# Kernel tuning notes

Hardware: AMD Instinct MI355X
Metric: run time of the kernel (lower is better)

## Reference

```python
import jax, jax.numpy as jnp
import numpy as np

B, T, F = 16, 4096, 80      # batch, frames, mel bins
C = 512                     # conv channels
ZD, ZN = 64, 512            # codebook dim / size
YD, YN = 128, 128           # speaker embed dim / count
K = 5                       # kernel size
SLOPE = 0.2                 # leaky relu negative slope


def conv1d(x, w, b):
    # x: [B,Cin,T], w: [Cout,Cin,K], 'same' padding, stride 1
    pad = (w.shape[-1] - 1) // 2
    y = jax.lax.conv_general_dilated(x, w, (1,), [(pad, pad)],
                                     dimension_numbers=('NCH', 'OIH', 'NCH'))
    return y + b[None, :, None]


def convT1(x, w, b):
    # torch ConvTranspose1d(stride=1, padding=(K-1)//2) == conv with spatially
    # flipped, in/out-swapped kernel. w: [Cin, Cout, K]
    wc = jnp.flip(w, -1).transpose(1, 0, 2)  # -> [Cout, Cin, K]
    return conv1d(x, wc, b)


def ln_c(x, g, b, eps=1e-5):
    # layer norm over channel axis, per (batch, time) position
    m = jnp.mean(x, 1, keepdims=True)
    v = jnp.var(x, 1, keepdims=True)
    return (x - m) * jax.lax.rsqrt(v + eps) * g[None, :, None] + b[None, :, None]


def _forward(x, y, enc_w1, enc_b1, enc_g1, enc_bt1, enc_w2, enc_b2, enc_g2, enc_bt2,
             enc_w3, enc_b3, enc_g3, enc_bt3, mlp_w, mlp_b, codebook, spk_emb,
             dec_w1, dec_b1, dec_g1, dec_bt1, dec_w2, dec_b2, dec_g2, dec_bt2,
             dec_w3, dec_b3):
    xc = x.transpose(0, 2, 1)                                    # [B,F,T]
    # Conditions: normalized speaker embedding lookup
    spk = spk_emb / jnp.linalg.norm(spk_emb, axis=1, keepdims=True)
    ye = spk[y].transpose(0, 2, 1)                               # [B,YD,T]
    # encoder: Conv1d -> LayerNorm(channel) -> LeakyReLU, x3, then 1x1 conv to z_dim
    h = jax.nn.leaky_relu(ln_c(conv1d(xc, enc_w1, enc_b1), enc_g1, enc_bt1), SLOPE)
    h = jax.nn.leaky_relu(ln_c(conv1d(h, enc_w2, enc_b2), enc_g2, enc_bt2), SLOPE)
    h = jax.nn.leaky_relu(ln_c(conv1d(h, enc_w3, enc_b3), enc_g3, enc_bt3), SLOPE)
    z = conv1d(h, mlp_w, mlp_b)                                  # [B,ZD,T]
    # vector quantizer (eval path): cdist^2 -> argmin -> gather
    zt = z.transpose(0, 2, 1)                                    # [B,T,ZD]
    zf = zt.reshape(-1, ZD)                                      # [B*T,ZD]
    d = (jnp.sum(zf * zf, axis=1, keepdims=True)
         + jnp.sum(codebook * codebook, axis=1)
         - 2.0 * zf @ codebook.T)                                # [B*T,ZN]
    idx = jnp.argmin(d, axis=1)
    z_vq = codebook[idx].reshape(zt.shape).transpose(0, 2, 1)    # [B,ZD,T]
    # decoder: (concat y -> ConvT -> LayerNorm -> GLU) x2, then concat y -> ConvT
    def glu_layer(h, w, b, g, bt):
        h = jnp.concatenate([h, ye], axis=1)
        h = ln_c(convT1(h, w, b), g, bt)
        a, gate = jnp.split(h, 2, axis=1)
        return a * jax.nn.sigmoid(gate)
    h = glu_layer(z_vq, dec_w1, dec_b1, dec_g1, dec_bt1)
    h = glu_layer(h, dec_w2, dec_b2, dec_g2, dec_bt2)
    h = jnp.concatenate([h, ye], axis=1)
    xhat = convT1(h, dec_w3, dec_b3)                             # [B,F,T]
    return xhat.transpose(0, 2, 1)                               # [B,T,F]


def setup_inputs() -> dict:
    key = jax.random.key(0)
    ks = jax.random.split(key, 16)
    def n(k, shape, sc=0.05):
        return jax.random.normal(k, shape, jnp.float32) * sc
    return {
        "x": jax.random.normal(ks[0], (B, T, F), jnp.float32),
        "y": jax.random.randint(ks[1], (B, T), 0, YN),
        "enc_w1": n(ks[2], (C, F, K)), "enc_b1": jnp.zeros(C), "enc_g1": jnp.ones(C), "enc_bt1": jnp.zeros(C),
        "enc_w2": n(ks[3], (C, C, K)), "enc_b2": jnp.zeros(C), "enc_g2": jnp.ones(C), "enc_bt2": jnp.zeros(C),
        "enc_w3": n(ks[4], (C, C, K)), "enc_b3": jnp.zeros(C), "enc_g3": jnp.ones(C), "enc_bt3": jnp.zeros(C),
        "mlp_w": n(ks[5], (ZD, C, 1)), "mlp_b": jnp.zeros(ZD),
        "codebook": jax.random.normal(ks[6], (ZN, ZD), jnp.float32),
        "spk_emb": jax.random.normal(ks[7], (YN, YD), jnp.float32),
        "dec_w1": n(ks[8], (ZD + YD, 2 * C, K)), "dec_b1": jnp.zeros(2 * C), "dec_g1": jnp.ones(2 * C), "dec_bt1": jnp.zeros(2 * C),
        "dec_w2": n(ks[9], (C + YD, 2 * C, K)), "dec_b2": jnp.zeros(2 * C), "dec_g2": jnp.ones(2 * C), "dec_bt2": jnp.zeros(2 * C),
        "dec_w3": n(ks[10], (C + YD, F, K)), "dec_b3": jnp.zeros(F),
    }


def reference(x, y, enc_w1, enc_b1, enc_g1, enc_bt1, enc_w2, enc_b2, enc_g2, enc_bt2,
              enc_w3, enc_b3, enc_g3, enc_bt3, mlp_w, mlp_b, codebook, spk_emb,
              dec_w1, dec_b1, dec_g1, dec_bt1, dec_w2, dec_b2, dec_g2, dec_bt2,
              dec_w3, dec_b3):
    return _forward(x, y, enc_w1, enc_b1, enc_g1, enc_bt1, enc_w2, enc_b2, enc_g2, enc_bt2,
                    enc_w3, enc_b3, enc_g3, enc_bt3, mlp_w, mlp_b, codebook, spk_emb,
                    dec_w1, dec_b1, dec_g1, dec_bt1, dec_w2, dec_b2, dec_g2, dec_bt2,
                    dec_w3, dec_b3)
```

## Files before the change

### kernel.cpp

```cpp
#include <hip/hip_runtime.h>
#include <hip/hip_bf16.h>
#include <cmath>

#define T_LEN 4096
#define BATCH 16
typedef __hip_bfloat16 bf16;
typedef unsigned short u16;
typedef float f32x4 __attribute__((ext_vector_type(4)));
typedef short s16x8 __attribute__((ext_vector_type(8)));

__device__ __forceinline__ float ldx(const void* p, int dt, size_t i) {
    return dt ? __bfloat162float(((const bf16*)p)[i]) : ((const float*)p)[i];
}
__device__ __forceinline__ void stx(void* p, int dt, size_t i, float v) {
    if (dt) ((bf16*)p)[i] = __float2bfloat16(v);
    else ((float*)p)[i] = v;
}
__device__ __forceinline__ u16 f2b(float v) {
    bf16 h = __float2bfloat16(v);
    return *(u16*)&h;
}
__device__ __forceinline__ float b2f(u16 u) {
    return __bfloat162float(*(const bf16*)&u);
}

__global__ void detect_kernel(const float* __restrict__ x, int* __restrict__ flag) {
    __shared__ int s[256];
    int tid = threadIdx.x;
    int bad = 0;
    for (int i = tid; i < 2048; i += 256) {
        float v = x[i];
        if (!(fabsf(v) < 1e30f)) bad = 1;
    }
    s[tid] = bad;
    __syncthreads();
    for (int off = 128; off > 0; off >>= 1) {
        if (tid < off) s[tid] |= s[tid + off];
        __syncthreads();
    }
    if (tid == 0) *flag = s[0];
}

__global__ void spk_norm_kernel(const int* __restrict__ dflag,
                                const void* __restrict__ spk,
                                float* __restrict__ out) {
    const int f = *dflag;
    int s = blockIdx.x, d = threadIdx.x;
    float v = ldx(spk, f, (size_t)s * 128 + d);
    __shared__ float red[128];
    red[d] = v * v;
    __syncthreads();
    for (int off = 64; off > 0; off >>= 1) {
        if (d < off) red[d] += red[d + off];
        __syncthreads();
    }
    float rs = rsqrtf(red[0]);
    out[s * 128 + d] = v * rs;
}

__global__ void repack_kernel(const int* __restrict__ dflag,
                              const void* __restrict__ src, int wmode,
                              int Cout, int Cin, int K, int ocp, int Cinp,
                              bf16* __restrict__ dsthi, bf16* __restrict__ dstlo) {
    const int F = *dflag;
    size_t total = (size_t)K * ocp * Cinp;
    size_t stride = (size_t)gridDim.x * 256;
    for (size_t i = (size_t)blockIdx.x * 256 + threadIdx.x; i < total; i += stride) {
        int k = (int)(i / ((size_t)ocp * Cinp));
        int r = (int)(i % ((size_t)ocp * Cinp));
        int oc = r / Cinp, ic = r % Cinp;
        float v = 0.f;
        if (oc < Cout && ic < Cin) {
            size_t off = wmode ? (((size_t)ic * Cout + oc) * K + (K - 1 - k))
                               : (((size_t)oc * Cin + ic) * K + k);
            v = ldx(src, F, off);
        }
        bf16 h = __float2bfloat16(v);
        dsthi[i] = h;
        if (dstlo) dstlo[i] = __float2bfloat16(v - __bfloat162float(h));
    }
}

__global__ void xprep_kernel(const int* __restrict__ dflag,
                             const void* __restrict__ x, int b0,
                             bf16* __restrict__ xp) {
    const int F = *dflag;
    int b = blockIdx.y;
    int t = blockIdx.x * 256 + threadIdx.x;
    size_t src = ((size_t)(b0 + b) * T_LEN + t) * 80;
    u16* row = (u16*)xp + ((size_t)b * T_LEN + t) * 192;
    for (int c4 = 0; c4 < 96; c4 += 4) {
        ushort4 h, l;
        u16* hp = (u16*)&h;
        u16* lp = (u16*)&l;
        for (int j = 0; j < 4; j++) {
            int c = c4 + j;
            float v = (c < 80) ? ldx(x, F, src + c) : 0.f;
            u16 hb = f2b(v);
            hp[j] = hb;
            lp[j] = f2b(v - b2f(hb));
        }
        *(ushort4*)&row[c4] = h;
        *(ushort4*)&row[96 + c4] = l;
    }
}

__global__ void ye_kernel(const int* __restrict__ y, int b0,
                          const float* __restrict__ spk_n,
                          bf16* __restrict__ D1, bf16* __restrict__ D2,
                          bf16* __restrict__ D3) {
    int b = blockIdx.y;
    int t = blockIdx.x * 256 + threadIdx.x;
    int idx = y[(size_t)(b0 + b) * T_LEN + t];
    const float* s = spk_n + (size_t)idx * 128;
    size_t r = (size_t)b * T_LEN + t;
    u16* p1 = (u16*)D1 + r * 192 + 64;
    u16* p2 = (u16*)D2 + r * 640 + 512;
    u16* p3 = (u16*)D3 + r * 640 + 512;
    for (int d4 = 0; d4 < 128; d4 += 4) {
        float4 v = *(const float4*)&s[d4];
        ushort4 h;
        h.x = f2b(v.x); h.y = f2b(v.y); h.z = f2b(v.z); h.w = f2b(v.w);
        *(ushort4*)&p1[d4] = h;
        *(ushort4*)&p2[d4] = h;
        *(ushort4*)&p3[d4] = h;
    }
}

template <int KK>
__global__ __launch_bounds__(256) void conv_mfma(
    const int* __restrict__ dflag,
    const bf16* __restrict__ act, int RS, int loOff, int aloMode, int Cinp,
    const bf16* __restrict__ whi, const bf16* __restrict__ wlo, int wloMode,
    const void* __restrict__ bias,
    void* __restrict__ outp, int odt, int oRS, int ocMax, int boff) {
    constexpr int PAD = (KK - 1) / 2;
    constexpr int SROWS = 128 + KK - 1;
    const int F = *dflag;
    const bool useALo = (aloMode == 1) || (aloMode == 2 && F == 0);
    const bool useWLo = (wloMode == 2 && F == 0) && (wlo != nullptr);
    const int ocp = gridDim.y << 6;
    const int t0 = blockIdx.x * 128;
    const int oc0 = blockIdx.y * 64;
    const int b = blockIdx.z;
    const int tid = threadIdx.x;
    const int lane = tid & 63;
    const int wid = tid >> 6;
    const int l16 = lane & 15;
    const int q8 = (lane >> 4) * 8;
    const int quad = lane >> 4;

    __shared__ __align__(16) bf16 sA[2 * SROWS * 40];
    __shared__ __align__(16) bf16 sB[KK * 64 * 40];

    f32x4 acc[2][4];
#pragma unroll
    for (int i = 0; i < 2; i++)
#pragma unroll
        for (int j = 0; j < 4; j++) acc[i][j] = (f32x4){0.f, 0.f, 0.f, 0.f};

    const int nch = Cinp >> 5;
    for (int ch = 0; ch < nch; ch++) {
        const int ic0 = ch << 5;
        for (int g = tid; g < SROWS * 8; g += 256) {
            int row = g >> 3, c4 = (g & 7) << 2;
            int t = t0 - PAD + row;
            ushort4 v = make_ushort4(0, 0, 0, 0);
            ushort4 vl = make_ushort4(0, 0, 0, 0);
            if (t >= 0 && t < T_LEN) {
                const u16* src = (const u16*)act + ((size_t)b * T_LEN + t) * RS + ic0 + c4;
                v = *(const ushort4*)src;
                if (useALo) vl = *(const ushort4*)(src + loOff);
            }
            *(ushort4*)&sA[row * 40 + c4] = v;
            if (useALo) *(ushort4*)&sA[(SROWS + row) * 40 + c4] = vl;
        }
        for (int g = tid; g < KK * 512; g += 256) {
            int tap = g >> 9;
            int rr = g & 511;
            int ocr = rr >> 3, c4 = (rr & 7) << 2;
            const u16* src = (const u16*)whi +
                             ((size_t)tap * ocp + oc0 + ocr) * Cinp + ic0 + c4;
            *(ushort4*)&sB[(tap * 64 + ocr) * 40 + c4] = *(const ushort4*)src;
        }
        __syncthreads();

#pragma unroll
        for (int tap = 0; tap < KK; tap++) {
            s16x8 bfr[4];
#pragma unroll
            for (int ni = 0; ni < 4; ni++)
                bfr[ni] = *(const s16x8*)&sB[(tap * 64 + ni * 16 + l16) * 40 + q8];
#pragma unroll
            for (int mi = 0; mi < 2; mi++) {
                int row = wid * 32 + mi * 16 + l16 + tap;
                s16x8 a = *(const s16x8*)&sA[row * 40 + q8];
#pragma unroll
                for (int ni = 0; ni < 4; ni++)
                    acc[mi][ni] = __builtin_amdgcn_mfma_f32_16x16x32_bf16(
                        a, bfr[ni], acc[mi][ni], 0, 0, 0);
                if (useALo) {
                    s16x8 al = *(const s16x8*)&sA[(SROWS + row) * 40 + q8];
#pragma unroll
                    for (int ni = 0; ni < 4; ni++)
                        acc[mi][ni] = __builtin_amdgcn_mfma_f32_16x16x32_bf16(
                            al, bfr[ni], acc[mi][ni], 0, 0, 0);
                }
            }
        }
        if (useWLo) {
            __syncthreads();
            for (int g = tid; g < KK * 512; g += 256) {
                int tap = g >> 9;
                int rr = g & 511;
                int ocr = rr >> 3, c4 = (rr & 7) << 2;
                const u16* src = (const u16*)wlo +
                                 ((size_t)tap * ocp + oc0 + ocr) * Cinp + ic0 + c4;
                *(ushort4*)&sB[(tap * 64 + ocr) * 40 + c4] = *(const ushort4*)src;
            }
            __syncthreads();
#pragma unroll
            for (int tap = 0; tap < KK; tap++) {
                s16x8 bfr[4];
#pragma unroll
                for (int ni = 0; ni < 4; ni++)
                    bfr[ni] = *(const s16x8*)&sB[(tap * 64 + ni * 16 + l16) * 40 + q8];
#pragma unroll
                for (int mi = 0; mi < 2; mi++) {
                    int row = wid * 32 + mi * 16 + l16 + tap;
                    s16x8 a = *(const s16x8*)&sA[row * 40 + q8];
#pragma unroll
                    for (int ni = 0; ni < 4; ni++)
                        acc[mi][ni] = __builtin_amdgcn_mfma_f32_16x16x32_bf16(
                            a, bfr[ni], acc[mi][ni], 0, 0, 0);
                }
            }
        }
        __syncthreads();
    }

#pragma unroll
    for (int ni = 0; ni < 4; ni++) {
        int oc = oc0 + ni * 16 + l16;
        if (oc >= ocMax) continue;
        float bv = ldx(bias, F, oc);
#pragma unroll
        for (int mi = 0; mi < 2; mi++) {
#pragma unroll
            for (int r = 0; r < 4; r++) {
                int t = t0 + wid * 32 + mi * 16 + quad * 4 + r;
                float v = acc[mi][ni][r] + bv;
                size_t off = ((size_t)(b + boff) * T_LEN + t) * (size_t)oRS + oc;
                if (odt == 0) ((float*)outp)[off] = v;
                else if (odt == 1) ((bf16*)outp)[off] = __float2bfloat16(v);
                else stx(outp, F, off, v);
            }
        }
    }
}

__global__ __launch_bounds__(256) void ln_lrelu(
    const int* __restrict__ dflag, const float* __restrict__ Fin,
    bf16* __restrict__ E, const void* __restrict__ g, const void* __restrict__ bt) {
    const int Fl = *dflag;
    int b = blockIdx.y;
    int t = blockIdx.x * 4 + (threadIdx.x >> 6);
    int lane = threadIdx.x & 63;
    const float* row = Fin + ((size_t)b * T_LEN + t) * 512 + lane * 8;
    float vv[8];
    *(float4*)&vv[0] = *(const float4*)row;
    *(float4*)&vv[4] = *(const float4*)(row + 4);
    float s = 0.f, s2 = 0.f;
#pragma unroll
    for (int j = 0; j < 8; j++) { s += vv[j]; s2 += vv[j] * vv[j]; }
    for (int m = 32; m; m >>= 1) {
        s += __shfl_xor(s, m);
        s2 += __shfl_xor(s2, m);
    }
    float mean = s / 512.f;
    float var = s2 / 512.f - mean * mean;
    float rstd = rsqrtf(var + 1e-5f);
    u16* eo = (u16*)E + ((size_t)b * T_LEN + t) * 1024 + lane * 8;
    ushort4 h[2], l[2];
#pragma unroll
    for (int j = 0; j < 8; j++) {
        int c = lane * 8 + j;
        float v = (vv[j] - mean) * rstd * ldx(g, Fl, c) + ldx(bt, Fl, c);
        v = v >= 0.f ? v : 0.2f * v;
        u16 hb = f2b(v);
        ((u16*)h)[j] = hb;
        ((u16*)l)[j] = f2b(v - b2f(hb));
    }
    *(ushort4*)&eo[0] = h[0];
    *(ushort4*)&eo[4] = h[1];
    *(ushort4*)&eo[512] = l[0];
    *(ushort4*)&eo[516] = l[1];
}

__global__ __launch_bounds__(256) void ln_glu(
    const int* __restrict__ dflag, const bf16* __restrict__ Fin,
    bf16* __restrict__ D, int oRS, const void* __restrict__ g,
    const void* __restrict__ bt) {
    const int Fl = *dflag;
    int b = blockIdx.y;
    int t = blockIdx.x * 4 + (threadIdx.x >> 6);
    int lane = threadIdx.x & 63;
    const u16* row = (const u16*)Fin + ((size_t)b * T_LEN + t) * 1024;
    ushort4 ua[2], ug[2];
    ua[0] = *(const ushort4*)&row[lane * 8];
    ua[1] = *(const ushort4*)&row[lane * 8 + 4];
    ug[0] = *(const ushort4*)&row[512 + lane * 8];
    ug[1] = *(const ushort4*)&row[512 + lane * 8 + 4];
    float av[8], gv[8];
#pragma unroll
    for (int j = 0; j < 8; j++) {
        av[j] = b2f(((u16*)ua)[j]);
        gv[j] = b2f(((u16*)ug)[j]);
    }
    float s = 0.f, s2 = 0.f;
#pragma unroll
    for (int j = 0; j < 8; j++) {
        s += av[j] + gv[j];
        s2 += av[j] * av[j] + gv[j] * gv[j];
    }
    for (int m = 32; m; m >>= 1) {
        s += __shfl_xor(s, m);
        s2 += __shfl_xor(s2, m);
    }
    float mean = s / 1024.f;
    float var = s2 / 1024.f - mean * mean;
    float rstd = rsqrtf(var + 1e-5f);
    ushort4 o[2];
#pragma unroll
    for (int j = 0; j < 8; j++) {
        int c = lane * 8 + j;
        float a = (av[j] - mean) * rstd * ldx(g, Fl, c) + ldx(bt, Fl, c);
        float gg = (gv[j] - mean) * rstd * ldx(g, Fl, 512 + c) + ldx(bt, Fl, 512 + c);
        ((u16*)o)[j] = f2b(a / (1.f + expf(-gg)));
    }
    u16* op = (u16*)D + ((size_t)b * T_LEN + t) * oRS + lane * 8;
    *(ushort4*)&op[0] = o[0];
    *(ushort4*)&op[4] = o[1];
}

__global__ __launch_bounds__(256) void vq_kernel(
    const int* __restrict__ dflag, const float* __restrict__ z,
    const void* __restrict__ cb, bf16* __restrict__ D1) {
    const int F = *dflag;
    int b = blockIdx.y;
    int t = blockIdx.x * 256 + threadIdx.x;
    int tid = threadIdx.x;

    __shared__ float sCB[128 * 64];
    __shared__ float sCC[128];

    float zr[64];
    const float* zp = z + ((size_t)b * T_LEN + t) * 64;
#pragma unroll
    for (int d4 = 0; d4 < 64; d4 += 4) *(float4*)&zr[d4] = *(const float4*)&zp[d4];
    float zz = 0.f;
#pragma unroll
    for (int d = 0; d < 64; d++) zz += zr[d] * zr[d];

    float best = 3.4e38f;
    int bidx = 0;
    for (int chunk = 0; chunk < 4; chunk++) {
        __syncthreads();
        for (int i = tid; i < 8192; i += 256)
            sCB[i] = ldx(cb, F, (size_t)chunk * 8192 + i);
        __syncthreads();
        if (tid < 128) {
            float cc = 0.f;
#pragma unroll 8
            for (int d = 0; d < 64; d++) {
                float cv = sCB[tid * 64 + d];
                cc += cv * cv;
            }
            sCC[tid] = cc;
        }
        __syncthreads();
        for (int c = 0; c < 128; c++) {
            const float* cp = &sCB[c * 64];
            float dot = 0.f;
#pragma unroll
            for (int d = 0; d < 64; d++) dot += zr[d] * cp[d];
            float dist = zz + sCC[c] - 2.f * dot;
            if (dist < best) { best = dist; bidx = chunk * 128 + c; }
        }
    }
    u16* out = (u16*)D1 + ((size_t)b * T_LEN + t) * 192;
    for (int d4 = 0; d4 < 64; d4 += 4) {
        ushort4 h;
        h.x = f2b(ldx(cb, F, (size_t)bidx * 64 + d4));
        h.y = f2b(ldx(cb, F, (size_t)bidx * 64 + d4 + 1));
        h.z = f2b(ldx(cb, F, (size_t)bidx * 64 + d4 + 2));
        h.w = f2b(ldx(cb, F, (size_t)bidx * 64 + d4 + 3));
        *(ushort4*)&out[d4] = h;
    }
}

extern "C" void kernel_launch(void* const* d_in, const int* in_sizes, int n_in,
                              void* d_out, int out_size, void* d_ws,
                              size_t ws_size, hipStream_t stream) {
    const void* x = d_in[0];
    const int* y = (const int*)d_in[1];
    const void* enc_w1 = d_in[2];  const void* enc_b1 = d_in[3];
    const void* enc_g1 = d_in[4];  const void* enc_bt1 = d_in[5];
    const void* enc_w2 = d_in[6];  const void* enc_b2 = d_in[7];
    const void* enc_g2 = d_in[8];  const void* enc_bt2 = d_in[9];
    const void* enc_w3 = d_in[10]; const void* enc_b3 = d_in[11];
    const void* enc_g3 = d_in[12]; const void* enc_bt3 = d_in[13];
    const void* mlp_w = d_in[14];  const void* mlp_b = d_in[15];
    const void* codebook = d_in[16];
    const void* spk_emb = d_in[17];
    const void* dec_w1 = d_in[18]; const void* dec_b1 = d_in[19];
    const void* dec_g1 = d_in[20]; const void* dec_bt1 = d_in[21];
    const void* dec_w2 = d_in[22]; const void* dec_b2 = d_in[23];
    const void* dec_g2 = d_in[24]; const void* dec_bt2 = d_in[25];
    const void* dec_w3 = d_in[26]; const void* dec_b3 = d_in[27];

    const size_t SW1 = (size_t)5 * 512 * 96;
    const size_t SW2 = (size_t)5 * 512 * 512;
    const size_t SW3 = SW2;
    const size_t SWM = (size_t)64 * 512;
    const size_t SD1 = (size_t)5 * 1024 * 192;
    const size_t SD2 = (size_t)5 * 1024 * 640;
    const size_t SD3 = (size_t)5 * 128 * 640;
    const size_t HI_TOT = SW1 + SW2 + SW3 + SWM + SD1 + SD2 + SD3;
    const size_t LO_TOT = SW1 + SW2 + SW3 + SWM;

    const size_t PB = (size_t)T_LEN * (192 * 2 + 1024 * 2 + 2048 + 64 * 4 + 640 * 2 + 640 * 2);
    const size_t FIXED = 256 + 65536 + (HI_TOT + LO_TOT) * 2;

    int nb = BATCH;
    while (nb > 1 && FIXED + (size_t)nb * PB > ws_size) nb >>= 1;

    char* p = (char*)d_ws;
    int* dflag = (int*)p;        p += 256;
    float* spk_n = (float*)p;    p += 65536;
    bf16* w1h = (bf16*)p;        p += SW1 * 2;
    bf16* w2h = (bf16*)p;        p += SW2 * 2;
    bf16* w3h = (bf16*)p;        p += SW3 * 2;
    bf16* wmh = (bf16*)p;        p += SWM * 2;
    bf16* wd1 = (bf16*)p;        p += SD1 * 2;
    bf16* wd2 = (bf16*)p;        p += SD2 * 2;
    bf16* wd3 = (bf16*)p;        p += SD3 * 2;
    bf16* w1l = (bf16*)p;        p += SW1 * 2;
    bf16* w2l = (bf16*)p;        p += SW2 * 2;
    bf16* w3l = (bf16*)p;        p += SW3 * 2;
    bf16* wml = (bf16*)p;        p += SWM * 2;
    bf16* xp = (bf16*)p;         p += (size_t)nb * T_LEN * 192 * 2;
    bf16* E = (bf16*)p;          p += (size_t)nb * T_LEN * 1024 * 2;
    char* Fb = p;                p += (size_t)nb * T_LEN * 2048;
    float* zbuf = (float*)p;     p += (size_t)nb * T_LEN * 64 * 4;
    bf16* D2 = (bf16*)p;         p += (size_t)nb * T_LEN * 640 * 2;
    bf16* D3 = (bf16*)p;
    bf16* D1 = xp;
    float* Ff = (float*)Fb;
    bf16* Fh = (bf16*)Fb;

    dim3 blk(256);

    detect_kernel<<<1, 256, 0, stream>>>((const float*)x, dflag);
    spk_norm_kernel<<<128, 128, 0, stream>>>(dflag, spk_emb, spk_n);

    repack_kernel<<<2048, blk, 0, stream>>>(dflag, enc_w1, 0, 512, 80, 5, 512, 96, w1h, w1l);
    repack_kernel<<<2048, blk, 0, stream>>>(dflag, enc_w2, 0, 512, 512, 5, 512, 512, w2h, w2l);
    repack_kernel<<<2048, blk, 0, stream>>>(dflag, enc_w3, 0, 512, 512, 5, 512, 512, w3h, w3l);
    repack_kernel<<<2048, blk, 0, stream>>>(dflag, mlp_w, 0, 64, 512, 1, 64, 512, wmh, wml);
    repack_kernel<<<2048, blk, 0, stream>>>(dflag, dec_w1, 1, 1024, 192, 5, 1024, 192, wd1, nullptr);
    repack_kernel<<<2048, blk, 0, stream>>>(dflag, dec_w2, 1, 1024, 640, 5, 1024, 640, wd2, nullptr);
    repack_kernel<<<2048, blk, 0, stream>>>(dflag, dec_w3, 1, 80, 640, 5, 128, 640, wd3, nullptr);

    for (int b0 = 0; b0 < BATCH; b0 += nb) {
        dim3 gT(T_LEN / 256, nb);
        dim3 gLN(T_LEN / 4, nb);

        xprep_kernel<<<gT, blk, 0, stream>>>(dflag, x, b0, xp);

        conv_mfma<5><<<dim3(32, 8, nb), blk, 0, stream>>>(
            dflag, xp, 192, 96, 2, 96, w1h, w1l, 2, enc_b1, Ff, 0, 512, 512, 0);
        ye_kernel<<<gT, blk, 0, stream>>>(y, b0, spk_n, D1, D2, D3);
        ln_lrelu<<<gLN, blk, 0, stream>>>(dflag, Ff, E, enc_g1, enc_bt1);
        conv_mfma<5><<<dim3(32, 8, nb), blk, 0, stream>>>(
            dflag, E, 1024, 512, 1, 512, w2h, w2l, 2, enc_b2, Ff, 0, 512, 512, 0);
        ln_lrelu<<<gLN, blk, 0, stream>>>(dflag, Ff, E, enc_g2, enc_bt2);
        conv_mfma<5><<<dim3(32, 8, nb), blk, 0, stream>>>(
            dflag, E, 1024, 512, 1, 512, w3h, w3l, 2, enc_b3, Ff, 0, 512, 512, 0);
        ln_lrelu<<<gLN, blk, 0, stream>>>(dflag, Ff, E, enc_g3, enc_bt3);

        conv_mfma<1><<<dim3(32, 1, nb), blk, 0, stream>>>(
            dflag, E, 1024, 512, 1, 512, wmh, wml, 2, mlp_b, zbuf, 0, 64, 64, 0);

        vq_kernel<<<gT, blk, 0, stream>>>(dflag, zbuf, codebook, D1);

        conv_mfma<5><<<dim3(32, 16, nb), blk, 0, stream>>>(
            dflag, D1, 192, 0, 0, 192, wd1, nullptr, 0, dec_b1, Fh, 1, 1024, 1024, 0);
        ln_glu<<<gLN, blk, 0, stream>>>(dflag, Fh, D2, 640, dec_g1, dec_bt1);
        conv_mfma<5><<<dim3(32, 16, nb), blk, 0, stream>>>(
            dflag, D2, 640, 0, 0, 640, wd2, nullptr, 0, dec_b2, Fh, 1, 1024, 1024, 0);
        ln_glu<<<gLN, blk, 0, stream>>>(dflag, Fh, D3, 640, dec_g2, dec_bt2);
        conv_mfma<5><<<dim3(32, 2, nb), blk, 0, stream>>>(
            dflag, D3, 640, 0, 0, 640, wd3, nullptr, 0, dec_b3, d_out, 2, 80, 80, b0);
    }
}
```

Measured before the change: 5.606 ms.

## Enlarge conv tile to 128 output channels, widen loads, tile weight repack

The MFMA conv kernel now computes 128 output channels per block instead of 64. The four waves are arranged 2x2 over time and channels, each holding a 64x64 accumulator tile, so every staged activation chunk is reused across twice as many channels. Global-to-LDS copies use 8-element vectors instead of 4, and the grids and padded weight sizes (the mlp weights pad to 128 rows) change to match. The weight repack kernels are split into forward and transposed variants that stage tiles in LDS so global writes are vectorized. In exchange, each thread holds twice the accumulator registers and the block uses more LDS, which can lower occupancy, and the grid has half as many blocks.

```diff
diff --git a/kernel.cpp b/kernel.cpp
--- a/kernel.cpp
+++ b/kernel.cpp
@@ -8,6 +8,7 @@
 typedef unsigned short u16;
 typedef float f32x4 __attribute__((ext_vector_type(4)));
 typedef short s16x8 __attribute__((ext_vector_type(8)));
+typedef unsigned short u16x8 __attribute__((ext_vector_type(8)));
 
 __device__ __forceinline__ float ldx(const void* p, int dt, size_t i) {
     return dt ? __bfloat162float(((const bf16*)p)[i]) : ((const float*)p)[i];
@@ -58,26 +59,81 @@
     out[s * 128 + d] = v * rs;
 }
 
-__global__ void repack_kernel(const int* __restrict__ dflag,
-                              const void* __restrict__ src, int wmode,
-                              int Cout, int Cin, int K, int ocp, int Cinp,
-                              bf16* __restrict__ dsthi, bf16* __restrict__ dstlo) {
+__global__ __launch_bounds__(256) void repack0_kernel(
+    const int* __restrict__ dflag, const void* __restrict__ src,
+    int Cout, int Cin, int K, int ocp, int Cinp,
+    bf16* __restrict__ dsthi, bf16* __restrict__ dstlo) {
     const int F = *dflag;
-    size_t total = (size_t)K * ocp * Cinp;
-    size_t stride = (size_t)gridDim.x * 256;
-    for (size_t i = (size_t)blockIdx.x * 256 + threadIdx.x; i < total; i += stride) {
-        int k = (int)(i / ((size_t)ocp * Cinp));
-        int r = (int)(i % ((size_t)ocp * Cinp));
-        int oc = r / Cinp, ic = r % Cinp;
+    __shared__ u16 sh[64 * 32 * 5];
+    __shared__ u16 sl[64 * 32 * 5];
+    const int ic0 = blockIdx.x * 32;
+    const int oc0 = blockIdx.y * 64;
+    const int tid = threadIdx.x;
+    const int N = 64 * 32 * K;
+    for (int idx = tid; idx < N; idx += 256) {
+        int ocl = idx / (32 * K);
+        int r = idx % (32 * K);
+        int icl = r / K, k = r % K;
+        int oc = oc0 + ocl, ic = ic0 + icl;
         float v = 0.f;
-        if (oc < Cout && ic < Cin) {
-            size_t off = wmode ? (((size_t)ic * Cout + oc) * K + (K - 1 - k))
-                               : (((size_t)oc * Cin + ic) * K + k);
-            v = ldx(src, F, off);
-        }
-        bf16 h = __float2bfloat16(v);
-        dsthi[i] = h;
-        if (dstlo) dstlo[i] = __float2bfloat16(v - __bfloat162float(h));
+        if (oc < Cout && ic < Cin)
+            v = ldx(src, F, ((size_t)oc * Cin + ic) * K + k);
+        u16 hb = f2b(v);
+        sh[(ocl * 32 + icl) * K + k] = hb;
+        sl[(ocl * 32 + icl) * K + k] = f2b(v - b2f(hb));
+    }
+    __syncthreads();
+    const int M = K * 64 * 4;
+    for (int idx = tid; idx < M; idx += 256) {
+        int k = idx / (64 * 4);
+        int r = idx % (64 * 4);
+        int ocl = r >> 2;
+        int g8 = (r & 3) << 3;
+        u16x8 h, l;
+#pragma unroll
+        for (int j = 0; j < 8; j++) {
+            h[j] = sh[(ocl * 32 + g8 + j) * K + k];
+            l[j] = sl[(ocl * 32 + g8 + j) * K + k];
+        }
+        size_t off = ((size_t)k * ocp + oc0 + ocl) * Cinp + ic0 + g8;
+        *(u16x8*)&dsthi[off] = h;
+        if (dstlo) *(u16x8*)&dstlo[off] = l;
+    }
+}
+
+__global__ __launch_bounds__(256) void repack1_kernel(
+    const int* __restrict__ dflag, const void* __restrict__ src,
+    int Cout, int Cin, int K, int ocp, int Cinp,
+    bf16* __restrict__ dsthi) {
+    const int F = *dflag;
+    __shared__ u16 sh[64 * 32 * 5];
+    const int ic0 = blockIdx.x * 64;
+    const int oc0 = blockIdx.y * 32;
+    const int tid = threadIdx.x;
+    const int N = 64 * 32 * K;
+    for (int idx = tid; idx < N; idx += 256) {
+        int icl = idx / (32 * K);
+        int r = idx % (32 * K);
+        int ocl = r / K, k = r % K;
+        int oc = oc0 + ocl, ic = ic0 + icl;
+        float v = 0.f;
+        if (oc < Cout && ic < Cin)
+            v = ldx(src, F, ((size_t)ic * Cout + oc) * K + k);
+        sh[(icl * 32 + ocl) * K + (K - 1 - k)] = f2b(v);
+    }
+    __syncthreads();
+    const int M = K * 32 * 8;
+    for (int idx = tid; idx < M; idx += 256) {
+        int k = idx / (32 * 8);
+        int r = idx % (32 * 8);
+        int ocl = r >> 3;
+        int g8 = (r & 7) << 3;
+        u16x8 h;
+#pragma unroll
+        for (int j = 0; j < 8; j++)
+            h[j] = sh[((g8 + j) * 32 + ocl) * K + k];
+        size_t off = ((size_t)k * ocp + oc0 + ocl) * Cinp + ic0 + g8;
+        *(u16x8*)&dsthi[off] = h;
     }
 }
 
@@ -139,49 +195,51 @@
     const int F = *dflag;
     const bool useALo = (aloMode == 1) || (aloMode == 2 && F == 0);
     const bool useWLo = (wloMode == 2 && F == 0) && (wlo != nullptr);
-    const int ocp = gridDim.y << 6;
+    const int ocp = gridDim.y << 7;
     const int t0 = blockIdx.x * 128;
-    const int oc0 = blockIdx.y * 64;
+    const int oc0 = blockIdx.y * 128;
     const int b = blockIdx.z;
     const int tid = threadIdx.x;
     const int lane = tid & 63;
     const int wid = tid >> 6;
+    const int widT = wid >> 1;
+    const int widN = wid & 1;
     const int l16 = lane & 15;
-    const int q8 = (lane >> 4) * 8;
     const int quad = lane >> 4;
+    const int q8 = quad * 8;
 
     __shared__ __align__(16) bf16 sA[2 * SROWS * 40];
-    __shared__ __align__(16) bf16 sB[KK * 64 * 40];
-
-    f32x4 acc[2][4];
-#pragma unroll
-    for (int i = 0; i < 2; i++)
+    __shared__ __align__(16) bf16 sB[KK * 128 * 40];
+
+    f32x4 acc[4][4];
+#pragma unroll
+    for (int i = 0; i < 4; i++)
 #pragma unroll
         for (int j = 0; j < 4; j++) acc[i][j] = (f32x4){0.f, 0.f, 0.f, 0.f};
 
     const int nch = Cinp >> 5;
     for (int ch = 0; ch < nch; ch++) {
         const int ic0 = ch << 5;
-        for (int g = tid; g < SROWS * 8; g += 256) {
-            int row = g >> 3, c4 = (g & 7) << 2;
+        for (int g = tid; g < SROWS * 4; g += 256) {
+            int row = g >> 2, c8 = (g & 3) << 3;
             int t = t0 - PAD + row;
-            ushort4 v = make_ushort4(0, 0, 0, 0);
-            ushort4 vl = make_ushort4(0, 0, 0, 0);
+            u16x8 v = (u16x8){0, 0, 0, 0, 0, 0, 0, 0};
+            u16x8 vl = (u16x8){0, 0, 0, 0, 0, 0, 0, 0};
             if (t >= 0 && t < T_LEN) {
-                const u16* src = (const u16*)act + ((size_t)b * T_LEN + t) * RS + ic0 + c4;
-                v = *(const ushort4*)src;
-                if (useALo) vl = *(const ushort4*)(src + loOff);
+                const u16* src = (const u16*)act + ((size_t)b * T_LEN + t) * RS + ic0 + c8;
+                v = *(const u16x8*)src;
+                if (useALo) vl = *(const u16x8*)(src + loOff);
             }
-            *(ushort4*)&sA[row * 40 + c4] = v;
-            if (useALo) *(ushort4*)&sA[(SROWS + row) * 40 + c4] = vl;
+            *(u16x8*)&sA[row * 40 + c8] = v;
+            if (useALo) *(u16x8*)&sA[(SROWS + row) * 40 + c8] = vl;
         }
         for (int g = tid; g < KK * 512; g += 256) {
             int tap = g >> 9;
-            int rr = g & 511;
-            int ocr = rr >> 3, c4 = (rr & 7) << 2;
+            int r = g & 511;
+            int ocr = r >> 2, c8 = (r & 3) << 3;
             const u16* src = (const u16*)whi +
-                             ((size_t)tap * ocp + oc0 + ocr) * Cinp + ic0 + c4;
-            *(ushort4*)&sB[(tap * 64 + ocr) * 40 + c4] = *(const ushort4*)src;
+                             ((size_t)tap * ocp + oc0 + ocr) * Cinp + ic0 + c8;
+            *(u16x8*)&sB[(tap * 128 + ocr) * 40 + c8] = *(const u16x8*)src;
         }
         __syncthreads();
 
@@ -190,10 +248,10 @@
             s16x8 bfr[4];
 #pragma unroll
             for (int ni = 0; ni < 4; ni++)
-                bfr[ni] = *(const s16x8*)&sB[(tap * 64 + ni * 16 + l16) * 40 + q8];
-#pragma unroll
-            for (int mi = 0; mi < 2; mi++) {
-                int row = wid * 32 + mi * 16 + l16 + tap;
+                bfr[ni] = *(const s16x8*)&sB[(tap * 128 + widN * 64 + ni * 16 + l16) * 40 + q8];
+#pragma unroll
+            for (int mi = 0; mi < 4; mi++) {
+                int row = widT * 64 + mi * 16 + l16 + tap;
                 s16x8 a = *(const s16x8*)&sA[row * 40 + q8];
 #pragma unroll
                 for (int ni = 0; ni < 4; ni++)
@@ -212,11 +270,11 @@
             __syncthreads();
             for (int g = tid; g < KK * 512; g += 256) {
                 int tap = g >> 9;
-                int rr = g & 511;
-                int ocr = rr >> 3, c4 = (rr & 7) << 2;
+                int r = g & 511;
+                int ocr = r >> 2, c8 = (r & 3) << 3;
                 const u16* src = (const u16*)wlo +
-                                 ((size_t)tap * ocp + oc0 + ocr) * Cinp + ic0 + c4;
-                *(ushort4*)&sB[(tap * 64 + ocr) * 40 + c4] = *(const ushort4*)src;
+                                 ((size_t)tap * ocp + oc0 + ocr) * Cinp + ic0 + c8;
+                *(u16x8*)&sB[(tap * 128 + ocr) * 40 + c8] = *(const u16x8*)src;
             }
             __syncthreads();
 #pragma unroll
@@ -224,10 +282,10 @@
                 s16x8 bfr[4];
 #pragma unroll
                 for (int ni = 0; ni < 4; ni++)
-                    bfr[ni] = *(const s16x8*)&sB[(tap * 64 + ni * 16 + l16) * 40 + q8];
-#pragma unroll
-                for (int mi = 0; mi < 2; mi++) {
-                    int row = wid * 32 + mi * 16 + l16 + tap;
+                    bfr[ni] = *(const s16x8*)&sB[(tap * 128 + widN * 64 + ni * 16 + l16) * 40 + q8];
+#pragma unroll
+                for (int mi = 0; mi < 4; mi++) {
+                    int row = widT * 64 + mi * 16 + l16 + tap;
                     s16x8 a = *(const s16x8*)&sA[row * 40 + q8];
 #pragma unroll
                     for (int ni = 0; ni < 4; ni++)
@@ -241,14 +299,14 @@
 
 #pragma unroll
     for (int ni = 0; ni < 4; ni++) {
-        int oc = oc0 + ni * 16 + l16;
+        int oc = oc0 + widN * 64 + ni * 16 + l16;
         if (oc >= ocMax) continue;
         float bv = ldx(bias, F, oc);
 #pragma unroll
-        for (int mi = 0; mi < 2; mi++) {
+        for (int mi = 0; mi < 4; mi++) {
 #pragma unroll
             for (int r = 0; r < 4; r++) {
-                int t = t0 + wid * 32 + mi * 16 + quad * 4 + r;
+                int t = t0 + widT * 64 + mi * 16 + quad * 4 + r;
                 float v = acc[mi][ni][r] + bv;
                 size_t off = ((size_t)(b + boff) * T_LEN + t) * (size_t)oRS + oc;
                 if (odt == 0) ((float*)outp)[off] = v;
@@ -422,7 +480,7 @@
     const size_t SW1 = (size_t)5 * 512 * 96;
     const size_t SW2 = (size_t)5 * 512 * 512;
     const size_t SW3 = SW2;
-    const size_t SWM = (size_t)64 * 512;
+    const size_t SWM = (size_t)128 * 512;
     const size_t SD1 = (size_t)5 * 1024 * 192;
     const size_t SD2 = (size_t)5 * 1024 * 640;
     const size_t SD3 = (size_t)5 * 128 * 640;
@@ -464,13 +522,13 @@
     detect_kernel<<<1, 256, 0, stream>>>((const float*)x, dflag);
     spk_norm_kernel<<<128, 128, 0, stream>>>(dflag, spk_emb, spk_n);
 
-    repack_kernel<<<2048, blk, 0, stream>>>(dflag, enc_w1, 0, 512, 80, 5, 512, 96, w1h, w1l);
-    repack_kernel<<<2048, blk, 0, stream>>>(dflag, enc_w2, 0, 512, 512, 5, 512, 512, w2h, w2l);
-    repack_kernel<<<2048, blk, 0, stream>>>(dflag, enc_w3, 0, 512, 512, 5, 512, 512, w3h, w3l);
-    repack_kernel<<<2048, blk, 0, stream>>>(dflag, mlp_w, 0, 64, 512, 1, 64, 512, wmh, wml);
-    repack_kernel<<<2048, blk, 0, stream>>>(dflag, dec_w1, 1, 1024, 192, 5, 1024, 192, wd1, nullptr);
-    repack_kernel<<<2048, blk, 0, stream>>>(dflag, dec_w2, 1, 1024, 640, 5, 1024, 640, wd2, nullptr);
-    repack_kernel<<<2048, blk, 0, stream>>>(dflag, dec_w3, 1, 80, 640, 5, 128, 640, wd3, nullptr);
+    repack0_kernel<<<dim3(3, 8), blk, 0, stream>>>(dflag, enc_w1, 512, 80, 5, 512, 96, w1h, w1l);
+    repack0_kernel<<<dim3(16, 8), blk, 0, stream>>>(dflag, enc_w2, 512, 512, 5, 512, 512, w2h, w2l);
+    repack0_kernel<<<dim3(16, 8), blk, 0, stream>>>(dflag, enc_w3, 512, 512, 5, 512, 512, w3h, w3l);
+    repack0_kernel<<<dim3(16, 2), blk, 0, stream>>>(dflag, mlp_w, 64, 512, 1, 128, 512, wmh, wml);
+    repack1_kernel<<<dim3(3, 32), blk, 0, stream>>>(dflag, dec_w1, 1024, 192, 5, 1024, 192, wd1);
+    repack1_kernel<<<dim3(10, 32), blk, 0, stream>>>(dflag, dec_w2, 1024, 640, 5, 1024, 640, wd2);
+    repack1_kernel<<<dim3(10, 4), blk, 0, stream>>>(dflag, dec_w3, 80, 640, 5, 128, 640, wd3);
 
     for (int b0 = 0; b0 < BATCH; b0 += nb) {
         dim3 gT(T_LEN / 256, nb);
@@ -478,14 +536,14 @@
 
         xprep_kernel<<<gT, blk, 0, stream>>>(dflag, x, b0, xp);
 
-        conv_mfma<5><<<dim3(32, 8, nb), blk, 0, stream>>>(
+        conv_mfma<5><<<dim3(32, 4, nb), blk, 0, stream>>>(
             dflag, xp, 192, 96, 2, 96, w1h, w1l, 2, enc_b1, Ff, 0, 512, 512, 0);
         ye_kernel<<<gT, blk, 0, stream>>>(y, b0, spk_n, D1, D2, D3);
         ln_lrelu<<<gLN, blk, 0, stream>>>(dflag, Ff, E, enc_g1, enc_bt1);
-        conv_mfma<5><<<dim3(32, 8, nb), blk, 0, stream>>>(
+        conv_mfma<5><<<dim3(32, 4, nb), blk, 0, stream>>>(
             dflag, E, 1024, 512, 1, 512, w2h, w2l, 2, enc_b2, Ff, 0, 512, 512, 0);
         ln_lrelu<<<gLN, blk, 0, stream>>>(dflag, Ff, E, enc_g2, enc_bt2);
-        conv_mfma<5><<<dim3(32, 8, nb), blk, 0, stream>>>(
+        conv_mfma<5><<<dim3(32, 4, nb), blk, 0, stream>>>(
             dflag, E, 1024, 512, 1, 512, w3h, w3l, 2, enc_b3, Ff, 0, 512, 512, 0);
         ln_lrelu<<<gLN, blk, 0, stream>>>(dflag, Ff, E, enc_g3, enc_bt3);
 
@@ -494,13 +552,13 @@
 
         vq_kernel<<<gT, blk, 0, stream>>>(dflag, zbuf, codebook, D1);
 
-        conv_mfma<5><<<dim3(32, 16, nb), blk, 0, stream>>>(
+        conv_mfma<5><<<dim3(32, 8, nb), blk, 0, stream>>>(
             dflag, D1, 192, 0, 0, 192, wd1, nullptr, 0, dec_b1, Fh, 1, 1024, 1024, 0);
         ln_glu<<<gLN, blk, 0, stream>>>(dflag, Fh, D2, 640, dec_g1, dec_bt1);
-        conv_mfma<5><<<dim3(32, 16, nb), blk, 0, stream>>>(
+        conv_mfma<5><<<dim3(32, 8, nb), blk, 0, stream>>>(
             dflag, D2, 640, 0, 0, 640, wd2, nullptr, 0, dec_b2, Fh, 1, 1024, 1024, 0);
         ln_glu<<<gLN, blk, 0, stream>>>(dflag, Fh, D3, 640, dec_g2, dec_bt2);
-        conv_mfma<5><<<dim3(32, 2, nb), blk, 0, stream>>>(
+        conv_mfma<5><<<dim3(32, 1, nb), blk, 0, stream>>>(
             dflag, D3, 640, 0, 0, 640, wd3, nullptr, 0, dec_b3, d_out, 2, 80, 80, b0);
     }
 }
```

Result: faster. 4.928 ms (-12.1%).
